# Performance work log

Measured on AMD Instinct MI355X. Metric: run time of the kernel, lower is better.

Reference implementation:

```python
import jax, jax.numpy as jnp
import numpy as np


def setup_inputs() -> dict:
    key = jax.random.key(0)
    k1, k2, k3 = jax.random.split(key, 3)
    B, L, D, KD = 4, 4096, 1024, 4096
    x = jax.random.normal(k1, (B, L, D), dtype=jnp.float32)
    k = jax.random.normal(k2, (D, KD), dtype=jnp.float32)
    skip = jax.random.normal(k3, (D,), dtype=jnp.float32)
    return {"x": x, "k": k, "skip": skip}


def reference(x, k, skip):
    # x: [B, L, D] -> transpose to [B, D, L] (channels-first, as in torch forward)
    xt = jnp.transpose(x, (0, 2, 1))
    L = xt.shape[-1]
    n = 2 * L  # zero-padded FFT length for linear (non-circular) convolution
    x_f = jnp.fft.rfft(xt, n=n)                 # [B, D, L+1] complex
    k_f = jnp.fft.rfft(k[:, :L], n=n)           # [D, L+1] complex
    y = jnp.fft.irfft(x_f * k_f, n=n)[..., :L]  # [B, D, L]
    # skip connection: per-channel scale of input
    y = y + xt * skip[None, :, None]
    return jnp.transpose(y, (0, 2, 1))          # back to [B, L, D]
```

## Files before the change

kernel.cpp:

```cpp
#include <hip/hip_runtime.h>


#define BB 4
#define LL 4096
#define DD 1024

typedef __attribute__((ext_vector_type(8))) short short8;
typedef __attribute__((ext_vector_type(16))) float f32x16;

__device__ __forceinline__ unsigned short f2bf(float f) {
    unsigned int u = __builtin_bit_cast(unsigned int, f);
    u += 0x7fffu + ((u >> 16) & 1u);
    return (unsigned short)(u >> 16);
}

__global__ __launch_bounds__(256) void transpose_x_bf16(const float* __restrict__ in,
                                                        unsigned short* __restrict__ out) {
    __shared__ float tile[32][33];
    int b = blockIdx.z;
    int c0 = blockIdx.x * 32;
    int r0 = blockIdx.y * 32;
    int tx = threadIdx.x, ty = threadIdx.y;
#pragma unroll
    for (int i = 0; i < 4; i++) {
        int r = r0 + ty + i * 8;
        tile[ty + i * 8][tx] = in[((size_t)b * LL + r) * DD + c0 + tx];
    }
    __syncthreads();
#pragma unroll
    for (int i = 0; i < 4; i++) {
        int c = c0 + ty + i * 8;
        out[((size_t)b * DD + c) * LL + r0 + tx] = f2bf(tile[tx][ty + i * 8]);
    }
}

__global__ __launch_bounds__(256) void transpose_y_skip(const float* __restrict__ yt,
                                                        const float* __restrict__ x,
                                                        const float* __restrict__ skip,
                                                        float* __restrict__ out) {
    __shared__ float tile[32][33];
    int b = blockIdx.z;
    int c0 = blockIdx.x * 32;
    int r0 = blockIdx.y * 32;
    int tx = threadIdx.x, ty = threadIdx.y;
#pragma unroll
    for (int i = 0; i < 4; i++) {
        int r = r0 + ty + i * 8;
        tile[ty + i * 8][tx] = yt[((size_t)b * DD + r) * LL + c0 + tx];
    }
    float sv = skip[r0 + tx];
    __syncthreads();
#pragma unroll
    for (int i = 0; i < 4; i++) {
        int c = c0 + ty + i * 8;
        size_t oi = ((size_t)b * LL + c) * DD + r0 + tx;
        out[oi] = tile[tx][ty + i * 8] + sv * x[oi];
    }
}

__global__ __launch_bounds__(512, 1) void conv_mfma(
        const unsigned short* __restrict__ xt,
        const float* __restrict__ kw,
        float* __restrict__ yt) {
    __shared__ unsigned int krev2x[4128];
    __shared__ unsigned char xbuf[34816];
    const int tid = threadIdx.x;
    const int lane = tid & 63;
    const int w = tid >> 6;
    const int lam = lane & 31;
    const int h = lane >> 5;

    for (int phase = 0; phase < 2; ++phase) {
        const int d = (blockIdx.x << 1) + phase;

        {
            const float* krow = kw + (size_t)d * LL;
            int j0 = tid << 3;
#pragma unroll
            for (int f = 0; f < 8; ++f) {
                int j = j0 + f;
                int i2 = 4094 - j;
                unsigned int lo = f2bf(krow[4095 - j]);
                unsigned int hi = (i2 >= 0) ? (unsigned int)f2bf(krow[i2]) : 0u;
                krev2x[j] = lo | (hi << 16);
            }
            if (tid < 32) krev2x[4096 + tid] = 0u;
        }
        for (int sid = tid; sid < 2176; sid += 512) {
            int c = sid >> 2, sraw = sid & 3;
            int J = c >> 2, b2 = c & 3;
            int ix = J - 8;
            uint4 v = {0u, 0u, 0u, 0u};
            if (ix >= 0)
                v = *(const uint4*)(xt + (((size_t)b2 * DD + d) * LL) + (ix << 5) + (sraw << 3));
            *(uint4*)(xbuf + (c << 6) + ((((sraw + c) & 3)) << 4)) = v;
        }
        __syncthreads();

        const int ta = w, tb = 15 - w;
        const int mmax_a = 8 * ta + 7;
        const int mmax_b = 8 * tb + 7;
        f32x16 acca, accb;
#pragma unroll
        for (int i = 0; i < 16; i++) { acca[i] = 0.f; accb[i] = 0.f; }

        for (int m = 0; m <= mmax_b; ++m) {
            const int c_a = ((8 + 8 * ta - m) << 2) + lam;
            const int c_b = ((8 + 8 * tb - m) << 2) + lam;
            const int a0m = 4095 - (m << 5) - lam + (h << 3);
#pragma unroll
            for (int q = 0; q < 2; ++q) {
                int a0 = a0m + (q << 4);
                unsigned int w0 = krev2x[a0];
                unsigned int w1 = krev2x[a0 + 2];
                unsigned int w2 = krev2x[a0 + 4];
                unsigned int w3 = krev2x[a0 + 6];
                struct U4 { unsigned int a, b, c, d; };
                U4 au{w0, w1, w2, w3};
                short8 af = __builtin_bit_cast(short8, au);
                int sq = (q << 1) + h;
                short8 bfb = *(const short8*)(xbuf + (c_b << 6) + ((((sq + c_b) & 3)) << 4));
                accb = __builtin_amdgcn_mfma_f32_32x32x16_bf16(af, bfb, accb, 0, 0, 0);
                if (m <= mmax_a) {
                    short8 bfa = *(const short8*)(xbuf + (c_a << 6) + ((((sq + c_a) & 3)) << 4));
                    acca = __builtin_amdgcn_mfma_f32_32x32x16_bf16(af, bfa, acca, 0, 0, 0);
                }
            }
        }
        __syncthreads();

        unsigned char* wr = xbuf + w * 4352;
#pragma unroll
        for (int tt = 0; tt < 2; ++tt) {
            int t = tt ? tb : ta;
            const f32x16& ac = tt ? accb : acca;
#pragma unroll
            for (int g = 0; g < 4; ++g) {
                float4 v = make_float4(ac[4 * g + 0], ac[4 * g + 1],
                                       ac[4 * g + 2], ac[4 * g + 3]);
                int sraw = (g << 1) + h;
                *(float4*)(wr + (lam << 7) + ((((sraw + lam) & 7)) << 4)) = v;
            }
#pragma unroll
            for (int j = 0; j < 4; ++j) {
                int colr = (lane >> 3) + (j << 3);
                int sr = lane & 7;
                float4 v = *(const float4*)(wr + (colr << 7) + ((((sr + colr) & 7)) << 4));
                int ii = (t << 3) + (colr >> 2);
                int b2 = colr & 3;
                *(float4*)(yt + (((size_t)b2 * DD + d) * LL) + (ii << 5) + (sr << 2)) = v;
            }
        }
        __syncthreads();
    }
}

#define NT 256
#define RPT 16
#define XS_PHYS 4368

__global__ __launch_bounds__(256) void conv_direct(
        const float* __restrict__ x_ld,
        const float* __restrict__ kw,
        const float* __restrict__ skip,
        float* __restrict__ out) {
    __shared__ float ks[LL];
    __shared__ float xs[XS_PHYS];
    int tid = threadIdx.x;
    int bid = blockIdx.x;
    int d = bid & (DD - 1);
    int b = bid >> 10;
    const float* krow = kw + (size_t)d * LL;
#pragma unroll
    for (int i = 0; i < LL; i += NT) ks[i + tid] = krow[i + tid];
    for (int i = tid; i < LL + 16; i += NT) {
        float v = (i < 16) ? 0.0f : x_ld[((size_t)b * LL + (i - 16)) * DD + d];
        xs[i + (i >> 4)] = v;
    }
    __syncthreads();
    float acc[RPT];
#pragma unroll
    for (int r = 0; r < RPT; r++) acc[r] = 0.0f;
#pragma unroll 1
    for (int c = 0; c <= tid; ++c) {
        int t0 = c << 4;
        float kk[16];
#pragma unroll
        for (int j = 0; j < 16; j++) kk[j] = ks[t0 + j];
        int pb = (tid - c) * 17 + 1;
        float xx[31];
#pragma unroll
        for (int u = 0; u < 31; u++) xx[u] = xs[pb + u + (u >= 15 ? 1 : 0)];
#pragma unroll
        for (int j = 0; j < 16; j++) {
#pragma unroll
            for (int r = 0; r < RPT; r++) acc[r] = fmaf(kk[j], xx[15 + r - j], acc[r]);
        }
    }
    float sk = skip[d];
    int pe = 17 * (tid + 1);
#pragma unroll
    for (int r = 0; r < RPT; r++) acc[r] = fmaf(sk, xs[pe + r], acc[r]);
    int l0 = tid << 4;
#pragma unroll
    for (int r = 0; r < RPT; r++)
        out[((size_t)b * LL + l0 + r) * DD + d] = acc[r];
}

extern "C" void kernel_launch(void* const* d_in, const int* in_sizes, int n_in,
                              void* d_out, int out_size, void* d_ws, size_t ws_size,
                              hipStream_t stream) {
    const float* x    = (const float*)d_in[0];
    const float* kw   = (const float*)d_in[1];
    const float* skip = (const float*)d_in[2];
    float* out = (float*)d_out;

    size_t xt_bytes = (size_t)BB * DD * LL * 2;
    size_t yt_bytes = (size_t)BB * DD * LL * 4;

    if (ws_size >= xt_bytes + yt_bytes) {
        unsigned short* xt = (unsigned short*)d_ws;
        float* yt = (float*)((char*)d_ws + xt_bytes);
        transpose_x_bf16<<<dim3(DD / 32, LL / 32, BB), dim3(32, 8), 0, stream>>>(x, xt);
        conv_mfma<<<dim3(DD / 2), dim3(512), 0, stream>>>(xt, kw, yt);
        transpose_y_skip<<<dim3(LL / 32, DD / 32, BB), dim3(32, 8), 0, stream>>>(yt, x, skip, out);
    } else {
        conv_direct<<<dim3(BB * DD), NT, 0, stream>>>(x, kw, skip, out);
    }
}
```

Baseline: 263.3 us.

## Rework conv and transpose kernels: one channel per block, register reuse, vectorized tiles

The MFMA convolution kernel now handles one channel per block instead of looping over two, which doubles the grid and raises launch bounds so more blocks can be resident. Each wave owns a pair of adjacent output tiles and carries x fragments in registers from one tile to the next, cutting shared-memory reads. The LDS layout uses an 80-byte padded stride in place of XOR swizzling, and results go straight to global memory without an LDS staging step. Both transpose kernels move to 64x64 tiles with float4 and 16-byte packed bf16 accesses, which adds register pressure and unroll complexity.

```diff
diff --git a/kernel.cpp b/kernel.cpp
--- a/kernel.cpp
+++ b/kernel.cpp
@@ -16,21 +16,32 @@
 
 __global__ __launch_bounds__(256) void transpose_x_bf16(const float* __restrict__ in,
                                                         unsigned short* __restrict__ out) {
-    __shared__ float tile[32][33];
+    __shared__ float tile[64][65];
     int b = blockIdx.z;
-    int c0 = blockIdx.x * 32;
-    int r0 = blockIdx.y * 32;
-    int tx = threadIdx.x, ty = threadIdx.y;
-#pragma unroll
-    for (int i = 0; i < 4; i++) {
-        int r = r0 + ty + i * 8;
-        tile[ty + i * 8][tx] = in[((size_t)b * LL + r) * DD + c0 + tx];
-    }
-    __syncthreads();
-#pragma unroll
-    for (int i = 0; i < 4; i++) {
-        int c = c0 + ty + i * 8;
-        out[((size_t)b * DD + c) * LL + r0 + tx] = f2bf(tile[tx][ty + i * 8]);
+    int d0 = blockIdx.x * 64;
+    int l0 = blockIdx.y * 64;
+    int tid = threadIdx.x;
+    int u = tid & 15, v = tid >> 4;
+#pragma unroll
+    for (int rr = 0; rr < 4; rr++) {
+        int l = v + 16 * rr;
+        float4 t4 = *(const float4*)&in[((size_t)b * LL + l0 + l) * DD + d0 + 4 * u];
+        tile[4 * u + 0][l] = t4.x;
+        tile[4 * u + 1][l] = t4.y;
+        tile[4 * u + 2][l] = t4.z;
+        tile[4 * u + 3][l] = t4.w;
+    }
+    __syncthreads();
+    int dd = tid & 63;
+    int jg = tid >> 6;
+#pragma unroll
+    for (int it = 0; it < 2; it++) {
+        int jj = jg + 4 * it;
+        unsigned short pk[8];
+#pragma unroll
+        for (int e = 0; e < 8; e++) pk[e] = f2bf(tile[dd][8 * jj + e]);
+        *(uint4*)&out[((size_t)b * DD + d0 + dd) * LL + l0 + 8 * jj] =
+            *(const uint4*)pk;
     }
 }
 
@@ -38,120 +49,147 @@
                                                         const float* __restrict__ x,
                                                         const float* __restrict__ skip,
                                                         float* __restrict__ out) {
-    __shared__ float tile[32][33];
+    __shared__ float tile[64][65];
     int b = blockIdx.z;
-    int c0 = blockIdx.x * 32;
-    int r0 = blockIdx.y * 32;
-    int tx = threadIdx.x, ty = threadIdx.y;
-#pragma unroll
-    for (int i = 0; i < 4; i++) {
-        int r = r0 + ty + i * 8;
-        tile[ty + i * 8][tx] = yt[((size_t)b * DD + r) * LL + c0 + tx];
-    }
-    float sv = skip[r0 + tx];
-    __syncthreads();
-#pragma unroll
-    for (int i = 0; i < 4; i++) {
-        int c = c0 + ty + i * 8;
-        size_t oi = ((size_t)b * LL + c) * DD + r0 + tx;
-        out[oi] = tile[tx][ty + i * 8] + sv * x[oi];
-    }
-}
-
-__global__ __launch_bounds__(512, 1) void conv_mfma(
+    int d0 = blockIdx.x * 64;
+    int l0 = blockIdx.y * 64;
+    int tid = threadIdx.x;
+    int u = tid & 15, v = tid >> 4;
+#pragma unroll
+    for (int rr = 0; rr < 4; rr++) {
+        int dd = v + 16 * rr;
+        float4 t4 = *(const float4*)&yt[((size_t)b * DD + d0 + dd) * LL + l0 + 4 * u];
+        tile[4 * u + 0][dd] = t4.x;
+        tile[4 * u + 1][dd] = t4.y;
+        tile[4 * u + 2][dd] = t4.z;
+        tile[4 * u + 3][dd] = t4.w;
+    }
+    __syncthreads();
+    int ug = tid & 15, lr = tid >> 4;
+    float4 sk4 = *(const float4*)&skip[d0 + 4 * ug];
+#pragma unroll
+    for (int rr = 0; rr < 4; rr++) {
+        int l = lr + 16 * rr;
+        size_t oi = ((size_t)b * LL + l0 + l) * DD + d0 + 4 * ug;
+        float4 x4 = *(const float4*)&x[oi];
+        float4 o4;
+        o4.x = tile[l][4 * ug + 0] + sk4.x * x4.x;
+        o4.y = tile[l][4 * ug + 1] + sk4.y * x4.y;
+        o4.z = tile[l][4 * ug + 2] + sk4.z * x4.z;
+        o4.w = tile[l][4 * ug + 3] + sk4.w * x4.w;
+        *(float4*)&out[oi] = o4;
+    }
+}
+
+__global__ __launch_bounds__(512, 4) void conv_mfma(
         const unsigned short* __restrict__ xt,
         const float* __restrict__ kw,
         float* __restrict__ yt) {
     __shared__ unsigned int krev2x[4128];
-    __shared__ unsigned char xbuf[34816];
+    __shared__ unsigned char xbuf[43520];
     const int tid = threadIdx.x;
     const int lane = tid & 63;
     const int w = tid >> 6;
     const int lam = lane & 31;
     const int h = lane >> 5;
-
-    for (int phase = 0; phase < 2; ++phase) {
-        const int d = (blockIdx.x << 1) + phase;
-
-        {
-            const float* krow = kw + (size_t)d * LL;
-            int j0 = tid << 3;
-#pragma unroll
-            for (int f = 0; f < 8; ++f) {
-                int j = j0 + f;
-                int i2 = 4094 - j;
-                unsigned int lo = f2bf(krow[4095 - j]);
-                unsigned int hi = (i2 >= 0) ? (unsigned int)f2bf(krow[i2]) : 0u;
-                krev2x[j] = lo | (hi << 16);
-            }
-            if (tid < 32) krev2x[4096 + tid] = 0u;
-        }
-        for (int sid = tid; sid < 2176; sid += 512) {
-            int c = sid >> 2, sraw = sid & 3;
-            int J = c >> 2, b2 = c & 3;
-            int ix = J - 8;
-            uint4 v = {0u, 0u, 0u, 0u};
-            if (ix >= 0)
-                v = *(const uint4*)(xt + (((size_t)b2 * DD + d) * LL) + (ix << 5) + (sraw << 3));
-            *(uint4*)(xbuf + (c << 6) + ((((sraw + c) & 3)) << 4)) = v;
-        }
-        __syncthreads();
-
-        const int ta = w, tb = 15 - w;
-        const int mmax_a = 8 * ta + 7;
-        const int mmax_b = 8 * tb + 7;
-        f32x16 acca, accb;
-#pragma unroll
-        for (int i = 0; i < 16; i++) { acca[i] = 0.f; accb[i] = 0.f; }
-
-        for (int m = 0; m <= mmax_b; ++m) {
-            const int c_a = ((8 + 8 * ta - m) << 2) + lam;
-            const int c_b = ((8 + 8 * tb - m) << 2) + lam;
-            const int a0m = 4095 - (m << 5) - lam + (h << 3);
-#pragma unroll
-            for (int q = 0; q < 2; ++q) {
-                int a0 = a0m + (q << 4);
-                unsigned int w0 = krev2x[a0];
-                unsigned int w1 = krev2x[a0 + 2];
-                unsigned int w2 = krev2x[a0 + 4];
-                unsigned int w3 = krev2x[a0 + 6];
+    const int d = blockIdx.x;
+
+    {
+        const float* krow = kw + (size_t)d * LL;
+        int j0 = tid << 3;
+#pragma unroll
+        for (int f = 0; f < 8; ++f) {
+            int j = j0 + f;
+            unsigned int lo = f2bf(krow[4095 - j]);
+            unsigned int hi = (j < 4095) ? (unsigned int)f2bf(krow[4094 - j]) : 0u;
+            krev2x[j] = lo | (hi << 16);
+        }
+        if (tid < 32) krev2x[4096 + tid] = 0u;
+    }
+    for (int sid = tid; sid < 2176; sid += 512) {
+        int c = sid >> 2, sr = sid & 3;
+        int J = c >> 2, b2 = c & 3;
+        int ix = J - 8;
+        uint4 v = {0u, 0u, 0u, 0u};
+        if (ix >= 0)
+            v = *(const uint4*)(xt + (((size_t)b2 * DD + d) * LL) + (ix << 5) + (sr << 3));
+        *(uint4*)(xbuf + c * 80 + sr * 16) = v;
+    }
+    __syncthreads();
+
+    const int p = (d & 1) ? (7 - w) : w;
+    const int t0 = 2 * p, t1 = 2 * p + 1;
+    const int nb = 2 * p + 2;
+
+    f32x16 acc0, acc1;
+#pragma unroll
+    for (int i = 0; i < 16; i++) { acc0[i] = 0.f; acc1[i] = 0.f; }
+
+#pragma unroll
+    for (int q = 0; q < 2; ++q) {
+        const int slot16 = (2 * q + h) * 16;
+        const int abase = 4095 - lam + 8 * h + 16 * q;
+        const unsigned char* xb = xbuf + lam * 80 + slot16;
+        short8 buf[8];
+
+#pragma unroll
+        for (int j = 0; j < 8; ++j) {
+            int m = j;
+            int a = abase - (m << 5);
+            unsigned int w0 = krev2x[a], w1 = krev2x[a + 2];
+            unsigned int w2 = krev2x[a + 4], w3 = krev2x[a + 6];
+            struct U4 { unsigned int a, b, c, d; };
+            U4 au{w0, w1, w2, w3};
+            short8 af = __builtin_bit_cast(short8, au);
+            short8 f0 = *(const short8*)(xb + (8 + 8 * t0 - m) * 320);
+            short8 f1 = *(const short8*)(xb + (8 + 8 * t1 - m) * 320);
+            acc0 = __builtin_amdgcn_mfma_f32_32x32x16_bf16(af, f0, acc0, 0, 0, 0);
+            acc1 = __builtin_amdgcn_mfma_f32_32x32x16_bf16(af, f1, acc1, 0, 0, 0);
+            buf[j] = f0;
+        }
+        for (int blk = 1; blk <= nb - 2; ++blk) {
+#pragma unroll
+            for (int j = 0; j < 8; ++j) {
+                int m = (blk << 3) + j;
+                int a = abase - (m << 5);
+                unsigned int w0 = krev2x[a], w1 = krev2x[a + 2];
+                unsigned int w2 = krev2x[a + 4], w3 = krev2x[a + 6];
                 struct U4 { unsigned int a, b, c, d; };
                 U4 au{w0, w1, w2, w3};
                 short8 af = __builtin_bit_cast(short8, au);
-                int sq = (q << 1) + h;
-                short8 bfb = *(const short8*)(xbuf + (c_b << 6) + ((((sq + c_b) & 3)) << 4));
-                accb = __builtin_amdgcn_mfma_f32_32x32x16_bf16(af, bfb, accb, 0, 0, 0);
-                if (m <= mmax_a) {
-                    short8 bfa = *(const short8*)(xbuf + (c_a << 6) + ((((sq + c_a) & 3)) << 4));
-                    acca = __builtin_amdgcn_mfma_f32_32x32x16_bf16(af, bfa, acca, 0, 0, 0);
-                }
+                short8 f0 = *(const short8*)(xb + (8 + 8 * t0 - m) * 320);
+                acc1 = __builtin_amdgcn_mfma_f32_32x32x16_bf16(af, buf[j], acc1, 0, 0, 0);
+                acc0 = __builtin_amdgcn_mfma_f32_32x32x16_bf16(af, f0, acc0, 0, 0, 0);
+                buf[j] = f0;
             }
         }
-        __syncthreads();
-
-        unsigned char* wr = xbuf + w * 4352;
-#pragma unroll
-        for (int tt = 0; tt < 2; ++tt) {
-            int t = tt ? tb : ta;
-            const f32x16& ac = tt ? accb : acca;
-#pragma unroll
-            for (int g = 0; g < 4; ++g) {
-                float4 v = make_float4(ac[4 * g + 0], ac[4 * g + 1],
-                                       ac[4 * g + 2], ac[4 * g + 3]);
-                int sraw = (g << 1) + h;
-                *(float4*)(wr + (lam << 7) + ((((sraw + lam) & 7)) << 4)) = v;
-            }
-#pragma unroll
-            for (int j = 0; j < 4; ++j) {
-                int colr = (lane >> 3) + (j << 3);
-                int sr = lane & 7;
-                float4 v = *(const float4*)(wr + (colr << 7) + ((((sr + colr) & 7)) << 4));
-                int ii = (t << 3) + (colr >> 2);
-                int b2 = colr & 3;
-                *(float4*)(yt + (((size_t)b2 * DD + d) * LL) + (ii << 5) + (sr << 2)) = v;
-            }
-        }
-        __syncthreads();
+#pragma unroll
+        for (int j = 0; j < 8; ++j) {
+            int m = ((nb - 1) << 3) + j;
+            int a = abase - (m << 5);
+            unsigned int w0 = krev2x[a], w1 = krev2x[a + 2];
+            unsigned int w2 = krev2x[a + 4], w3 = krev2x[a + 6];
+            struct U4 { unsigned int a, b, c, d; };
+            U4 au{w0, w1, w2, w3};
+            short8 af = __builtin_bit_cast(short8, au);
+            acc1 = __builtin_amdgcn_mfma_f32_32x32x16_bf16(af, buf[j], acc1, 0, 0, 0);
+        }
+    }
+
+    const int b2 = lam & 3;
+    const int j2 = lam >> 2;
+#pragma unroll
+    for (int tt = 0; tt < 2; ++tt) {
+        int t = tt ? t1 : t0;
+        const f32x16& ac = tt ? acc1 : acc0;
+        int i = 8 * t + j2;
+        float* base = yt + (((size_t)b2 * DD + d) * LL) + (i << 5) + 4 * h;
+#pragma unroll
+        for (int g = 0; g < 4; ++g) {
+            float4 v = make_float4(ac[4 * g + 0], ac[4 * g + 1],
+                                   ac[4 * g + 2], ac[4 * g + 3]);
+            *(float4*)(base + 8 * g) = v;
+        }
     }
 }
 
@@ -183,10 +221,10 @@
     for (int r = 0; r < RPT; r++) acc[r] = 0.0f;
 #pragma unroll 1
     for (int c = 0; c <= tid; ++c) {
-        int t0 = c << 4;
+        int tt0 = c << 4;
         float kk[16];
 #pragma unroll
-        for (int j = 0; j < 16; j++) kk[j] = ks[t0 + j];
+        for (int j = 0; j < 16; j++) kk[j] = ks[tt0 + j];
         int pb = (tid - c) * 17 + 1;
         float xx[31];
 #pragma unroll
@@ -221,9 +259,9 @@
     if (ws_size >= xt_bytes + yt_bytes) {
         unsigned short* xt = (unsigned short*)d_ws;
         float* yt = (float*)((char*)d_ws + xt_bytes);
-        transpose_x_bf16<<<dim3(DD / 32, LL / 32, BB), dim3(32, 8), 0, stream>>>(x, xt);
-        conv_mfma<<<dim3(DD / 2), dim3(512), 0, stream>>>(xt, kw, yt);
-        transpose_y_skip<<<dim3(LL / 32, DD / 32, BB), dim3(32, 8), 0, stream>>>(yt, x, skip, out);
+        transpose_x_bf16<<<dim3(DD / 64, LL / 64, BB), dim3(256), 0, stream>>>(x, xt);
+        conv_mfma<<<dim3(DD), dim3(512), 0, stream>>>(xt, kw, yt);
+        transpose_y_skip<<<dim3(DD / 64, LL / 64, BB), dim3(256), 0, stream>>>(yt, x, skip, out);
     } else {
         conv_direct<<<dim3(BB * DD), NT, 0, stream>>>(x, kw, skip, out);
     }
```

Result: faster. 225.5 us (-14.4%).
